# Optimization experiments

Measured on AMD Instinct MI355X. Metric: run time of the kernel, lower is better.

## Reference

```python
import jax, jax.numpy as jnp
import numpy as np

B = 262144
IN = 89          # obs(39) + one-hot task(50)
H = 64           # hidden_size
OUT = 8          # output_size
T = 50           # num_tasks


def setup_inputs() -> dict:
    key = jax.random.key(0)
    ks = jax.random.split(key, 10)
    s = 1.0 / np.sqrt(H)
    inputs = jax.random.normal(ks[0], (B, IN), dtype=jnp.float32)
    task_indices = jax.random.randint(ks[1], (B,), 0, T, dtype=jnp.int32)
    # trunk: 3 Linear+Tanh layers
    W0 = jax.random.normal(ks[2], (IN, H), dtype=jnp.float32) / np.sqrt(IN)
    b0 = jnp.zeros((H,), dtype=jnp.float32)
    W1 = jax.random.normal(ks[3], (H, H), dtype=jnp.float32) * s
    b1 = jnp.zeros((H,), dtype=jnp.float32)
    W2 = jax.random.normal(ks[4], (H, H), dtype=jnp.float32) * s
    b2 = jnp.zeros((H,), dtype=jnp.float32)
    # per-task output heads: num_task_layers=1 -> single Linear (no tanh)
    head_W = jax.random.normal(ks[5], (T, H, OUT), dtype=jnp.float32) * s
    head_b = jnp.zeros((T, OUT), dtype=jnp.float32)
    return {"inputs": inputs, "task_indices": task_indices,
            "W0": W0, "b0": b0, "W1": W1, "b1": b1, "W2": W2, "b2": b2,
            "head_W": head_W, "head_b": head_b}


def reference(inputs, task_indices, W0, b0, W1, b1, W2, b2, head_W, head_b):
    # Shared trunk: Linear + Tanh x3
    h = jnp.tanh(inputs @ W0 + b0)   # [B, H]
    h = jnp.tanh(h @ W1 + b1)
    h = jnp.tanh(h @ W2 + b2)
    # MoE-style dispatch/combine: gather per-sample head weights and apply.
    # Mathematically identical to partitioning by task, applying each head,
    # and scattering results back to original order.
    Wg = head_W[task_indices]        # [B, H, OUT]
    bg = head_b[task_indices]        # [B, OUT]
    out = jnp.einsum('bh,bho->bo', h, Wg) + bg  # [B, OUT]
    return out
```

## Files before the change

kernel.cpp:

```cpp
#include <hip/hip_runtime.h>
#include <stdint.h>
#include <stddef.h>


typedef _Float16 half8 __attribute__((ext_vector_type(8)));
typedef _Float16 half4 __attribute__((ext_vector_type(4)));
typedef _Float16 half2v __attribute__((ext_vector_type(2)));
typedef float    f32x4 __attribute__((ext_vector_type(4)));

constexpr int BN = 262144, INF = 89, HID = 64, OUTF = 8, NTASK = 50;
constexpr int NTHR = 128;
constexpr int ROWS = 64;
constexpr int XP   = 104;

constexpr int W0F_OFF = 0;
constexpr int W1F_OFF = 12288;
constexpr int W2F_OFF = 20480;
constexpr int HWT_OFF = 28672;

__device__ __forceinline__ float fast_tanh(float v) {
    float e = __expf(2.0f * v);
    return 1.0f - 2.0f * __builtin_amdgcn_rcpf(e + 1.0f);
}

__device__ __forceinline__ float dot2acc(half2v a, half2v b, float c) {
#if __has_builtin(__builtin_amdgcn_fdot2)
    return __builtin_amdgcn_fdot2(a, b, c, false);
#else
    return fmaf((float)a[0], (float)b[0], fmaf((float)a[1], (float)b[1], c));
#endif
}

__global__ void prep_kernel(const float* __restrict__ W0, const float* __restrict__ W1,
                            const float* __restrict__ W2, const float* __restrict__ hW,
                            _Float16* __restrict__ ws) {
    const int tid = blockIdx.x * blockDim.x + threadIdx.x;
    const int stride = gridDim.x * blockDim.x;
    _Float16* w0f = ws + W0F_OFF / 2;
    _Float16* w1f = ws + W1F_OFF / 2;
    _Float16* w2f = ws + W2F_OFF / 2;
    _Float16* hwt = ws + HWT_OFF / 2;
    for (int i = tid; i < 3 * 4 * 64 * 8; i += stride) {
        int j = i & 7, l = (i >> 3) & 63, fk = i >> 9;
        int kk = fk >> 2, ft = fk & 3;
        int n = ft * 16 + (l & 15);
        int k = kk * 32 + (l >> 4) * 8 + j;
        w0f[i] = (_Float16)(k < INF ? W0[k * HID + n] : 0.0f);
    }
    for (int i = tid; i < 2 * 4 * 64 * 8; i += stride) {
        int j = i & 7, l = (i >> 3) & 63, fk = i >> 9;
        int kk = fk >> 2, ft = fk & 3;
        int n = ft * 16 + (l & 15);
        int k = kk * 32 + (l >> 4) * 8 + j;
        w1f[i] = (_Float16)W1[k * HID + n];
        w2f[i] = (_Float16)W2[k * HID + n];
    }
    for (int i = tid; i < NTASK * OUTF * HID; i += stride) {
        int t = i / (OUTF * HID), rem = i % (OUTF * HID);
        int o = rem / HID, k = rem % HID;
        hwt[i] = (_Float16)hW[(size_t)t * (HID * OUTF) + k * OUTF + o];
    }
}

__global__ __launch_bounds__(NTHR, 8) void mtn_mfma_kernel(
    const float* __restrict__ x,
    const int*   __restrict__ task,
    const float* __restrict__ b0, const float* __restrict__ b1,
    const float* __restrict__ b2,
    const float* __restrict__ hB,
    const _Float16* __restrict__ ws,
    float* __restrict__ out)
{
    __shared__ __align__(16) _Float16 xh[ROWS * XP];

    const int t = threadIdx.x;
    const int w = t >> 6;
    const int l = t & 63;
    const int c = l & 15;
    const int g = l >> 4;
    const int blockRow = blockIdx.x * ROWS;
    const int waveRow  = w * 32;

    const _Float16* w0f = ws + W0F_OFF / 2;
    const _Float16* w1f = ws + W1F_OFF / 2;
    const _Float16* w2f = ws + W2F_OFF / 2;
    const _Float16* hwt = ws + HWT_OFF / 2;

    const int jr = l >> 3, jo = l & 7;
    int   tks[4];
    float hBv[4];
    #pragma unroll
    for (int it = 0; it < 4; ++it)
        tks[it] = task[blockRow + waveRow + it * 8 + jr];
    #pragma unroll
    for (int it = 0; it < 4; ++it)
        hBv[it] = hB[tks[it] * OUTF + jo];

    {
        const float* xw = x + (size_t)(blockRow + waveRow) * INF;
        #pragma unroll
        for (int i = 0; i < 11; ++i) {
            const int f   = l + i * 64;
            const int row = f / 22;
            const int c4  = f - row * 22;
            float4 v = *reinterpret_cast<const float4*>(xw + row * INF + c4 * 4);
            half4 hv = {(_Float16)v.x, (_Float16)v.y, (_Float16)v.z, (_Float16)v.w};
            *(half4*)&xh[(waveRow + row) * XP + c4 * 4] = hv;
        }
        if (l < 32) {
            const float v88 = xw[l * INF + 88];
            half4 t88 = {(_Float16)v88, (_Float16)0, (_Float16)0, (_Float16)0};
            half4 z4  = {(_Float16)0, (_Float16)0, (_Float16)0, (_Float16)0};
            *(half4*)&xh[(waveRow + l) * XP + 88] = t88;
            *(half4*)&xh[(waveRow + l) * XP + 92] = z4;
        }
    }

    f32x4 acc[4][2];

    #pragma unroll
    for (int ft = 0; ft < 4; ++ft) {
        f32x4 bv = *(const f32x4*)(b0 + ft * 16 + g * 4);
        acc[ft][0] = bv; acc[ft][1] = bv;
    }
    #pragma unroll
    for (int kk = 0; kk < 3; ++kk) {
        half8 bf[2];
        #pragma unroll
        for (int bt = 0; bt < 2; ++bt)
            bf[bt] = *(const half8*)&xh[(waveRow + bt * 16 + c) * XP + kk * 32 + g * 8];
        #pragma unroll
        for (int ft = 0; ft < 4; ++ft) {
            half8 af = *(const half8*)(w0f + ((kk * 4 + ft) * 64 + l) * 8);
            acc[ft][0] = __builtin_amdgcn_mfma_f32_16x16x32_f16(af, bf[0], acc[ft][0], 0, 0, 0);
            acc[ft][1] = __builtin_amdgcn_mfma_f32_16x16x32_f16(af, bf[1], acc[ft][1], 0, 0, 0);
        }
    }
    #pragma unroll
    for (int ft = 0; ft < 4; ++ft)
        #pragma unroll
        for (int bt = 0; bt < 2; ++bt) {
            half4 hv;
            #pragma unroll
            for (int r = 0; r < 4; ++r) hv[r] = (_Float16)fast_tanh(acc[ft][bt][r]);
            *(half4*)&xh[(waveRow + bt * 16 + c) * XP + ft * 16 + g * 4] = hv;
        }

    #pragma unroll
    for (int layer = 0; layer < 2; ++layer) {
        const _Float16* WF  = layer ? w2f : w1f;
        const float*    bia = layer ? b2  : b1;
        #pragma unroll
        for (int ft = 0; ft < 4; ++ft) {
            f32x4 bv = *(const f32x4*)(bia + ft * 16 + g * 4);
            acc[ft][0] = bv; acc[ft][1] = bv;
        }
        #pragma unroll
        for (int kk = 0; kk < 2; ++kk) {
            half8 bf[2];
            #pragma unroll
            for (int bt = 0; bt < 2; ++bt)
                bf[bt] = *(const half8*)&xh[(waveRow + bt * 16 + c) * XP + kk * 32 + g * 8];
            #pragma unroll
            for (int ft = 0; ft < 4; ++ft) {
                half8 af = *(const half8*)(WF + ((kk * 4 + ft) * 64 + l) * 8);
                acc[ft][0] = __builtin_amdgcn_mfma_f32_16x16x32_f16(af, bf[0], acc[ft][0], 0, 0, 0);
                acc[ft][1] = __builtin_amdgcn_mfma_f32_16x16x32_f16(af, bf[1], acc[ft][1], 0, 0, 0);
            }
        }
        #pragma unroll
        for (int ft = 0; ft < 4; ++ft)
            #pragma unroll
            for (int bt = 0; bt < 2; ++bt) {
                half4 hv;
                #pragma unroll
                for (int r = 0; r < 4; ++r) hv[r] = (_Float16)fast_tanh(acc[ft][bt][r]);
                *(half4*)&xh[(waveRow + bt * 16 + c) * XP + ft * 16 + g * 4] = hv;
            }
    }

    #pragma unroll
    for (int it = 0; it < 4; ++it) {
        const int r = it * 8 + jr;
        const size_t grow = (size_t)blockRow + waveRow + r;
        const int tk = tks[it];
        const _Float16* wp = hwt + (size_t)tk * (OUTF * HID) + jo * 8;
        const half8 hv = *(const half8*)&xh[(waveRow + r) * XP + jo * 8];

        float p[8];
        #pragma unroll
        for (int o = 0; o < 8; ++o) {
            half8 wv = *(const half8*)(wp + o * HID);
            float a = 0.0f;
            #pragma unroll
            for (int pp = 0; pp < 4; ++pp) {
                half2v av = {hv[2 * pp], hv[2 * pp + 1]};
                half2v bv = {wv[2 * pp], wv[2 * pp + 1]};
                a = dot2acc(av, bv, a);
            }
            p[o] = a;
        }
        float t0 = p[0] + __shfl_xor(p[0], 1);
        float t1 = p[1] + __shfl_xor(p[1], 1);
        float t2 = p[2] + __shfl_xor(p[2], 1);
        float t3 = p[3] + __shfl_xor(p[3], 1);
        float t4 = p[4] + __shfl_xor(p[4], 1);
        float t5 = p[5] + __shfl_xor(p[5], 1);
        float t6 = p[6] + __shfl_xor(p[6], 1);
        float t7 = p[7] + __shfl_xor(p[7], 1);
        const bool b0s = (jo & 1) != 0;
        float s0 = b0s ? t1 : t0;
        float s1 = b0s ? t3 : t2;
        float s2 = b0s ? t5 : t4;
        float s3 = b0s ? t7 : t6;
        s0 += __shfl_xor(s0, 2);
        s1 += __shfl_xor(s1, 2);
        s2 += __shfl_xor(s2, 2);
        s3 += __shfl_xor(s3, 2);
        const bool b1s = (jo & 2) != 0;
        float u0 = b1s ? s1 : s0;
        float u1 = b1s ? s3 : s2;
        u0 += __shfl_xor(u0, 4);
        u1 += __shfl_xor(u1, 4);
        float res = ((jo & 4) ? u1 : u0) + hBv[it];
        out[grow * OUTF + jo] = res;
    }
}

extern "C" void kernel_launch(void* const* d_in, const int* in_sizes, int n_in,
                              void* d_out, int out_size, void* d_ws, size_t ws_size,
                              hipStream_t stream) {
    const float* x    = (const float*)d_in[0];
    const int*   task = (const int*)  d_in[1];
    const float* W0   = (const float*)d_in[2];
    const float* b0   = (const float*)d_in[3];
    const float* W1   = (const float*)d_in[4];
    const float* b1   = (const float*)d_in[5];
    const float* W2   = (const float*)d_in[6];
    const float* b2   = (const float*)d_in[7];
    const float* hW   = (const float*)d_in[8];
    const float* hB   = (const float*)d_in[9];
    float* out = (float*)d_out;
    _Float16* ws = (_Float16*)d_ws;

    prep_kernel<<<64, 256, 0, stream>>>(W0, W1, W2, hW, ws);
    mtn_mfma_kernel<<<BN / ROWS, NTHR, 0, stream>>>(x, task, b0, b1, b2, hB, ws, out);
}
```

Before: 44.66 us.

## Process two row tiles per block with register prefetch of the second tile

```diff
diff --git a/kernel.cpp b/kernel.cpp
--- a/kernel.cpp
+++ b/kernel.cpp
@@ -9,9 +9,10 @@
 typedef float    f32x4 __attribute__((ext_vector_type(4)));
 
 constexpr int BN = 262144, INF = 89, HID = 64, OUTF = 8, NTASK = 50;
-constexpr int NTHR = 128;
-constexpr int ROWS = 64;
-constexpr int XP   = 104;
+constexpr int NTHR  = 128;
+constexpr int TROWS = 64;
+constexpr int NT    = 2;
+constexpr int XP    = 104;
 
 constexpr int W0F_OFF = 0;
 constexpr int W1F_OFF = 12288;
@@ -62,60 +63,47 @@
     }
 }
 
-__global__ __launch_bounds__(NTHR, 8) void mtn_mfma_kernel(
-    const float* __restrict__ x,
-    const int*   __restrict__ task,
+__device__ __forceinline__ void stage_load(const float* __restrict__ xw, int l,
+                                           float4 v[11], float& v88) {
+    #pragma unroll
+    for (int i = 0; i < 11; ++i) {
+        const int f   = l + i * 64;
+        const int row = f / 22;
+        const int c4  = f - row * 22;
+        v[i] = *reinterpret_cast<const float4*>(xw + row * INF + c4 * 4);
+    }
+    if (l < 32) v88 = xw[l * INF + 88];
+}
+
+__device__ __forceinline__ void stage_store(_Float16* __restrict__ band, int l,
+                                            const float4 v[11], float v88) {
+    #pragma unroll
+    for (int i = 0; i < 11; ++i) {
+        const int f   = l + i * 64;
+        const int row = f / 22;
+        const int c4  = f - row * 22;
+        half4 hv = {(_Float16)v[i].x, (_Float16)v[i].y,
+                    (_Float16)v[i].z, (_Float16)v[i].w};
+        *(half4*)&band[row * XP + c4 * 4] = hv;
+    }
+    if (l < 32) {
+        half4 t88 = {(_Float16)v88, (_Float16)0, (_Float16)0, (_Float16)0};
+        half4 z4  = {(_Float16)0, (_Float16)0, (_Float16)0, (_Float16)0};
+        *(half4*)&band[l * XP + 88] = t88;
+        *(half4*)&band[l * XP + 92] = z4;
+    }
+}
+
+__device__ __forceinline__ void compute_tile(
+    _Float16* __restrict__ band,
+    const _Float16* __restrict__ w0f, const _Float16* __restrict__ w1f,
+    const _Float16* __restrict__ w2f, const _Float16* __restrict__ hwt,
     const float* __restrict__ b0, const float* __restrict__ b1,
     const float* __restrict__ b2,
-    const float* __restrict__ hB,
-    const _Float16* __restrict__ ws,
-    float* __restrict__ out)
+    const int* tks, const float* hBv,
+    size_t growBase, int l, float* __restrict__ out)
 {
-    __shared__ __align__(16) _Float16 xh[ROWS * XP];
-
-    const int t = threadIdx.x;
-    const int w = t >> 6;
-    const int l = t & 63;
-    const int c = l & 15;
-    const int g = l >> 4;
-    const int blockRow = blockIdx.x * ROWS;
-    const int waveRow  = w * 32;
-
-    const _Float16* w0f = ws + W0F_OFF / 2;
-    const _Float16* w1f = ws + W1F_OFF / 2;
-    const _Float16* w2f = ws + W2F_OFF / 2;
-    const _Float16* hwt = ws + HWT_OFF / 2;
-
-    const int jr = l >> 3, jo = l & 7;
-    int   tks[4];
-    float hBv[4];
-    #pragma unroll
-    for (int it = 0; it < 4; ++it)
-        tks[it] = task[blockRow + waveRow + it * 8 + jr];
-    #pragma unroll
-    for (int it = 0; it < 4; ++it)
-        hBv[it] = hB[tks[it] * OUTF + jo];
-
-    {
-        const float* xw = x + (size_t)(blockRow + waveRow) * INF;
-        #pragma unroll
-        for (int i = 0; i < 11; ++i) {
-            const int f   = l + i * 64;
-            const int row = f / 22;
-            const int c4  = f - row * 22;
-            float4 v = *reinterpret_cast<const float4*>(xw + row * INF + c4 * 4);
-            half4 hv = {(_Float16)v.x, (_Float16)v.y, (_Float16)v.z, (_Float16)v.w};
-            *(half4*)&xh[(waveRow + row) * XP + c4 * 4] = hv;
-        }
-        if (l < 32) {
-            const float v88 = xw[l * INF + 88];
-            half4 t88 = {(_Float16)v88, (_Float16)0, (_Float16)0, (_Float16)0};
-            half4 z4  = {(_Float16)0, (_Float16)0, (_Float16)0, (_Float16)0};
-            *(half4*)&xh[(waveRow + l) * XP + 88] = t88;
-            *(half4*)&xh[(waveRow + l) * XP + 92] = z4;
-        }
-    }
-
+    const int c = l & 15, g = l >> 4, jr = l >> 3, jo = l & 7;
     f32x4 acc[4][2];
 
     #pragma unroll
@@ -128,7 +116,7 @@
         half8 bf[2];
         #pragma unroll
         for (int bt = 0; bt < 2; ++bt)
-            bf[bt] = *(const half8*)&xh[(waveRow + bt * 16 + c) * XP + kk * 32 + g * 8];
+            bf[bt] = *(const half8*)&band[(bt * 16 + c) * XP + kk * 32 + g * 8];
         #pragma unroll
         for (int ft = 0; ft < 4; ++ft) {
             half8 af = *(const half8*)(w0f + ((kk * 4 + ft) * 64 + l) * 8);
@@ -143,7 +131,7 @@
             half4 hv;
             #pragma unroll
             for (int r = 0; r < 4; ++r) hv[r] = (_Float16)fast_tanh(acc[ft][bt][r]);
-            *(half4*)&xh[(waveRow + bt * 16 + c) * XP + ft * 16 + g * 4] = hv;
+            *(half4*)&band[(bt * 16 + c) * XP + ft * 16 + g * 4] = hv;
         }
 
     #pragma unroll
@@ -160,7 +148,7 @@
             half8 bf[2];
             #pragma unroll
             for (int bt = 0; bt < 2; ++bt)
-                bf[bt] = *(const half8*)&xh[(waveRow + bt * 16 + c) * XP + kk * 32 + g * 8];
+                bf[bt] = *(const half8*)&band[(bt * 16 + c) * XP + kk * 32 + g * 8];
             #pragma unroll
             for (int ft = 0; ft < 4; ++ft) {
                 half8 af = *(const half8*)(WF + ((kk * 4 + ft) * 64 + l) * 8);
@@ -175,17 +163,17 @@
                 half4 hv;
                 #pragma unroll
                 for (int r = 0; r < 4; ++r) hv[r] = (_Float16)fast_tanh(acc[ft][bt][r]);
-                *(half4*)&xh[(waveRow + bt * 16 + c) * XP + ft * 16 + g * 4] = hv;
+                *(half4*)&band[(bt * 16 + c) * XP + ft * 16 + g * 4] = hv;
             }
     }
 
     #pragma unroll
     for (int it = 0; it < 4; ++it) {
         const int r = it * 8 + jr;
-        const size_t grow = (size_t)blockRow + waveRow + r;
+        const size_t grow = growBase + r;
         const int tk = tks[it];
         const _Float16* wp = hwt + (size_t)tk * (OUTF * HID) + jo * 8;
-        const half8 hv = *(const half8*)&xh[(waveRow + r) * XP + jo * 8];
+        const half8 hv = *(const half8*)&band[r * XP + jo * 8];
 
         float p[8];
         #pragma unroll
@@ -222,9 +210,59 @@
         float u1 = b1s ? s3 : s2;
         u0 += __shfl_xor(u0, 4);
         u1 += __shfl_xor(u1, 4);
-        float res = ((jo & 4) ? u1 : u0) + hBv[it];
-        out[grow * OUTF + jo] = res;
-    }
+        out[grow * OUTF + jo] = ((jo & 4) ? u1 : u0) + hBv[it];
+    }
+}
+
+__global__ __launch_bounds__(NTHR, 3) void mtn_mfma_kernel(
+    const float* __restrict__ x,
+    const int*   __restrict__ task,
+    const float* __restrict__ b0, const float* __restrict__ b1,
+    const float* __restrict__ b2,
+    const float* __restrict__ hB,
+    const _Float16* __restrict__ ws,
+    float* __restrict__ out)
+{
+    __shared__ __align__(16) _Float16 xh[NT][TROWS * XP];
+
+    const int t = threadIdx.x;
+    const int w = t >> 6;
+    const int l = t & 63;
+    const int jr = l >> 3, jo = l & 7;
+    const int blockRow = blockIdx.x * (TROWS * NT);
+    const int waveRow  = w * 32;
+
+    const _Float16* w0f = ws + W0F_OFF / 2;
+    const _Float16* w1f = ws + W1F_OFF / 2;
+    const _Float16* w2f = ws + W2F_OFF / 2;
+    const _Float16* hwt = ws + HWT_OFF / 2;
+
+    int   tks[8];
+    float hBv[8];
+    #pragma unroll
+    for (int it = 0; it < 4; ++it) {
+        tks[it]     = task[blockRow + waveRow + it * 8 + jr];
+        tks[4 + it] = task[blockRow + TROWS + waveRow + it * 8 + jr];
+    }
+    #pragma unroll
+    for (int it = 0; it < 8; ++it)
+        hBv[it] = hB[tks[it] * OUTF + jo];
+
+    const float* xw0 = x + (size_t)(blockRow + waveRow) * INF;
+    const float* xw1 = x + (size_t)(blockRow + TROWS + waveRow) * INF;
+    _Float16* band0 = &xh[0][waveRow * XP];
+    _Float16* band1 = &xh[1][waveRow * XP];
+
+    float4 v0[11], v1[11];
+    float  v880 = 0.0f, v881 = 0.0f;
+    stage_load(xw0, l, v0, v880);
+    stage_store(band0, l, v0, v880);
+    stage_load(xw1, l, v1, v881);
+    compute_tile(band0, w0f, w1f, w2f, hwt, b0, b1, b2,
+                 tks, hBv, (size_t)blockRow + waveRow, l, out);
+    stage_store(band1, l, v1, v881);
+    compute_tile(band1, w0f, w1f, w2f, hwt, b0, b1, b2,
+                 tks + 4, hBv + 4, (size_t)blockRow + TROWS + waveRow, l, out);
 }
 
 extern "C" void kernel_launch(void* const* d_in, const int* in_sizes, int n_in,
@@ -244,5 +282,6 @@
     _Float16* ws = (_Float16*)d_ws;
 
     prep_kernel<<<64, 256, 0, stream>>>(W0, W1, W2, hW, ws);
-    mtn_mfma_kernel<<<BN / ROWS, NTHR, 0, stream>>>(x, task, b0, b1, b2, hB, ws, out);
-}
+    mtn_mfma_kernel<<<BN / (TROWS * NT), NTHR, 0, stream>>>(x, task, b0, b1, b2,
+                                                            hB, ws, out);
+}
```

Result: slower. 109.5 us (+145.1%).
